# Optimization experiments

Hardware: AMD Instinct MI355X
Metric: run time of the kernel (lower is better)

## Reference

```python
import jax, jax.numpy as jnp
import numpy as np

N_NODES = 100000
N_EDGES = 3200000
HIDDEN = 64
OUT = 30


def _graph_conv(x, src, dst, W, b, n_nodes):
    # DGL GraphConv with norm='both': D_out^{-1/2} -> aggregate -> D_in^{-1/2} -> W -> +b
    ones = jnp.ones(src.shape[0], dtype=x.dtype)
    deg_out = jax.ops.segment_sum(ones, src, num_segments=n_nodes)
    deg_in = jax.ops.segment_sum(ones, dst, num_segments=n_nodes)
    norm_out = jnp.where(deg_out > 0, jax.lax.rsqrt(jnp.maximum(deg_out, 1e-30)), 0.0)
    norm_in = jnp.where(deg_in > 0, jax.lax.rsqrt(jnp.maximum(deg_in, 1e-30)), 0.0)
    h = x * norm_out[:, None]                    # [N, F] scaled source features
    msg = h[src]                                 # [E, F] gather
    agg = jax.ops.segment_sum(msg, dst, num_segments=n_nodes)  # [N, F] scatter-add
    agg = agg * norm_in[:, None]
    return agg @ W + b


def setup_inputs() -> dict:
    key = jax.random.key(0)
    k1, k2, k3, k4, k5 = jax.random.split(key, 5)
    x = jax.random.normal(k1, (N_NODES, HIDDEN), dtype=jnp.float32)
    src = jax.random.randint(k2, (N_EDGES,), 0, N_NODES, dtype=jnp.int32)
    dst = jax.random.randint(k3, (N_EDGES,), 0, N_NODES, dtype=jnp.int32)
    W1 = jax.random.normal(k4, (HIDDEN, HIDDEN), dtype=jnp.float32) / np.sqrt(HIDDEN)
    b1 = jnp.zeros((HIDDEN,), dtype=jnp.float32)
    W2 = jax.random.normal(k5, (HIDDEN, OUT), dtype=jnp.float32) / np.sqrt(HIDDEN)
    b2 = jnp.zeros((OUT,), dtype=jnp.float32)
    return {"x": x, "src": src, "dst": dst, "W1": W1, "b1": b1, "W2": W2, "b2": b2}


def reference(x, src, dst, W1, b1, W2, b2):
    h = _graph_conv(x, src, dst, W1, b1, N_NODES)
    h = jax.nn.relu(h)                           # conv1 activation=F.relu
    out = _graph_conv(h, src, dst, W2, b2, N_NODES)  # conv2: no activation
    return out
```

## Files before the change

kernel.cpp:

```cpp
#include <hip/hip_runtime.h>


#define NN 100000
#define NE 3200000
#define NOUTF 30
#define TPB 256
#define TPBW 1024
#define TPBS 1024

#define DSH 7
#define DCB 128
#define DNB ((NN + DCB - 1) / DCB)
#define SSH 8
#define SCB 256
#define SNB ((NN + SCB - 1) / SCB)

#define CHUNK 8192
#define NBLK ((NE + CHUNK - 1) / CHUNK)
#define HLD (DNB * NBLK)
#define HLS (SNB * NBLK)
#define HLT (HLD + HLS)
#define EPT (CHUNK / TPBS)

#define GCH 1024
#define NSC ((HLT + GCH - 1) / GCH)

#define POOL 4608

__device__ __forceinline__ unsigned short f2bf(float f) {
  unsigned u = __float_as_uint(f);
  u = (u + 0x7FFFu + ((u >> 16) & 1u)) >> 16;
  return (unsigned short)u;
}

__device__ __forceinline__ void acc8(float* a, const uint4& u) {
  a[0] += __uint_as_float(u.x << 16);
  a[1] += __uint_as_float(u.x & 0xFFFF0000u);
  a[2] += __uint_as_float(u.y << 16);
  a[3] += __uint_as_float(u.y & 0xFFFF0000u);
  a[4] += __uint_as_float(u.z << 16);
  a[5] += __uint_as_float(u.z & 0xFFFF0000u);
  a[6] += __uint_as_float(u.w << 16);
  a[7] += __uint_as_float(u.w & 0xFFFF0000u);
}

__device__ __forceinline__ int xcd_swz(int orig, int n) {
  int q = n / 8, r = n % 8;
  int xcd = orig % 8, idx = orig / 8;
  return (xcd < r ? xcd * (q + 1) : r * (q + 1) + (xcd - r) * q) + idx;
}

__global__ __launch_bounds__(TPBW) void k_hist(const int* __restrict__ src,
                                               const int* __restrict__ dst,
                                               int* __restrict__ H) {
  __shared__ int hd[DNB], hs[SNB];
  int t = threadIdx.x, k = blockIdx.x;
  for (int b = t; b < DNB; b += TPBW) hd[b] = 0;
  for (int b = t; b < SNB; b += TPBW) hs[b] = 0;
  __syncthreads();
  int beg = k * CHUNK, end = min(NE, beg + CHUNK);
  for (int i = beg + t; i < end; i += TPBW) {
    atomicAdd(&hd[dst[i] >> DSH], 1);
    atomicAdd(&hs[src[i] >> SSH], 1);
  }
  __syncthreads();
  for (int b = t; b < DNB; b += TPBW) H[b * NBLK + k] = hd[b];
  for (int b = t; b < SNB; b += TPBW) H[HLD + b * NBLK + k] = hs[b];
}

__global__ __launch_bounds__(TPB) void g_scan1(const int* __restrict__ a,
                                               int* __restrict__ bsums) {
  int t = threadIdx.x;
  int base = blockIdx.x * GCH + t * 4;
  int s = 0;
#pragma unroll
  for (int j = 0; j < 4; ++j) { int idx = base + j; if (idx < HLT) s += a[idx]; }
  __shared__ int red[TPB];
  red[t] = s; __syncthreads();
  for (int off = TPB / 2; off > 0; off >>= 1) {
    if (t < off) red[t] += red[t + off];
    __syncthreads();
  }
  if (t == 0) bsums[blockIdx.x] = red[0];
}

__global__ __launch_bounds__(1024) void g_scan2(int* __restrict__ bsums) {
  int t = threadIdx.x;
  __shared__ int lds[1024];
  int v = (t < NSC) ? bsums[t] : 0;
  int acc = v; lds[t] = acc; __syncthreads();
  for (int off = 1; off < 1024; off <<= 1) {
    int add = (t >= off) ? lds[t - off] : 0; __syncthreads();
    acc += add; lds[t] = acc; __syncthreads();
  }
  if (t < NSC) bsums[t] = acc - v;
}

__global__ __launch_bounds__(TPB) void g_scan3(int* __restrict__ a,
                                               const int* __restrict__ bsums) {
  int t = threadIdx.x;
  int base = blockIdx.x * GCH + t * 4;
  int v[4]; int s = 0;
#pragma unroll
  for (int j = 0; j < 4; ++j) {
    int idx = base + j;
    v[j] = (idx < HLT) ? a[idx] : 0;
    s += v[j];
  }
  __shared__ int lds[TPB];
  int acc = s; lds[t] = acc; __syncthreads();
  for (int off = 1; off < TPB; off <<= 1) {
    int add = (t >= off) ? lds[t - off] : 0; __syncthreads();
    acc += add; lds[t] = acc; __syncthreads();
  }
  int run = bsums[blockIdx.x] + (acc - s);
#pragma unroll
  for (int j = 0; j < 4; ++j) {
    int idx = base + j;
    if (idx < HLT) a[idx] = run;
    run += v[j];
  }
}

__global__ __launch_bounds__(TPBS) void k_scatter(const int* __restrict__ src,
                                                  const int* __restrict__ dst,
                                                  const int* __restrict__ Hsc,
                                                  int* __restrict__ packed,
                                                  unsigned char* __restrict__ ss) {
  __shared__ unsigned short perm_d[CHUNK];
  __shared__ unsigned short perm_s[CHUNK];
  __shared__ int baseD[DNB + 1], curD[DNB];
  __shared__ int baseS[SNB + 1], curS[SNB];
  __shared__ int scanbuf[TPBS];
  int t = threadIdx.x;
  int k = xcd_swz((int)blockIdx.x, NBLK);
  int beg = k * CHUNK, end = min(NE, beg + CHUNK);
  int cnt = end - beg;

  int es[EPT], ed[EPT];
#pragma unroll
  for (int j = 0; j < EPT; ++j) {
    int i = beg + j * TPBS + t;
    if (i < end) { es[j] = src[i]; ed[j] = dst[i]; }
    else { es[j] = -1; ed[j] = -1; }
  }

  for (int b = t; b < DNB; b += TPBS) curD[b] = 0;
  for (int b = t; b < SNB; b += TPBS) curS[b] = 0;
  __syncthreads();
#pragma unroll
  for (int j = 0; j < EPT; ++j) {
    if (ed[j] >= 0) {
      atomicAdd(&curD[ed[j] >> DSH], 1);
      atomicAdd(&curS[es[j] >> SSH], 1);
    }
  }
  __syncthreads();

  {
    int v = (t < DNB) ? curD[t] : 0;
    int acc = v; scanbuf[t] = acc; __syncthreads();
    for (int off = 1; off < TPBS; off <<= 1) {
      int add = (t >= off) ? scanbuf[t - off] : 0; __syncthreads();
      acc += add; scanbuf[t] = acc; __syncthreads();
    }
    if (t < DNB) baseD[t] = acc - v;
    if (t == 0) baseD[DNB] = cnt;
  }
  __syncthreads();
  {
    int v = (t < SNB) ? curS[t] : 0;
    int acc = v; scanbuf[t] = acc; __syncthreads();
    for (int off = 1; off < TPBS; off <<= 1) {
      int add = (t >= off) ? scanbuf[t - off] : 0; __syncthreads();
      acc += add; scanbuf[t] = acc; __syncthreads();
    }
    if (t < SNB) baseS[t] = acc - v;
    if (t == 0) baseS[SNB] = cnt;
  }
  __syncthreads();
  for (int b = t; b < DNB; b += TPBS) curD[b] = baseD[b];
  for (int b = t; b < SNB; b += TPBS) curS[b] = baseS[b];
  __syncthreads();

#pragma unroll
  for (int j = 0; j < EPT; ++j) {
    if (ed[j] >= 0) {
      int li = j * TPBS + t;
      int p = atomicAdd(&curD[ed[j] >> DSH], 1);
      perm_d[p] = (unsigned short)li;
      int q = atomicAdd(&curS[es[j] >> SSH], 1);
      perm_s[q] = (unsigned short)li;
    }
  }
  __syncthreads();

  for (int i = t; i < cnt; i += TPBS) {
    int gi = beg + perm_d[i];
    int d = dst[gi], s = src[gi];
    int bkt = d >> DSH;
    packed[Hsc[bkt * NBLK + k] + (i - baseD[bkt])] = (s << DSH) | (d & (DCB - 1));
  }
  for (int i = t; i < cnt; i += TPBS) {
    int gi = beg + perm_s[i];
    int s = src[gi];
    int bkt = s >> SSH;
    ss[Hsc[HLD + bkt * NBLK + k] + (i - baseS[bkt]) - NE] = (unsigned char)(s & (SCB - 1));
  }
}

__global__ __launch_bounds__(TPB) void k_fine_sort(const int* __restrict__ Hsc,
                                                   const int* __restrict__ packed,
                                                   int* __restrict__ src_sorted,
                                                   int* __restrict__ row_ptr,
                                                   float* __restrict__ norm_in) {
  __shared__ int hist[DCB], scn[DCB], cur[DCB];
  __shared__ int pool[POOL];
  int t = threadIdx.x, b = blockIdx.x;
  int seg_beg = Hsc[b * NBLK];
  int seg_end = (b + 1 < DNB) ? Hsc[(b + 1) * NBLK] : NE;
  int cnt = seg_end - seg_beg;
  if (t < DCB) hist[t] = 0;
  __syncthreads();
  for (int i = seg_beg + t; i < seg_end; i += TPB)
    atomicAdd(&hist[packed[i] & (DCB - 1)], 1);
  __syncthreads();
  if (t < DCB) scn[t] = hist[t];
  __syncthreads();
  for (int off = 1; off < DCB; off <<= 1) {
    int add = (t >= off && t < DCB) ? scn[t - off] : 0;
    __syncthreads();
    if (t < DCB) scn[t] += add;
    __syncthreads();
  }
  if (t < DCB) {
    int excl = scn[t] - hist[t];
    cur[t] = excl;
    int node = b * DCB + t;
    if (node < NN) {
      row_ptr[node] = seg_beg + excl;
      norm_in[node] = (hist[t] > 0) ? rsqrtf((float)hist[t]) : 0.0f;
    }
  }
  if (b == DNB - 1 && t == 0) row_ptr[NN] = NE;
  __syncthreads();
  for (int i = seg_beg + t; i < seg_end; i += TPB) {
    int v = packed[i];
    int p = atomicAdd(&cur[v & (DCB - 1)], 1);
    int sv = v >> DSH;
    if (p < POOL) pool[p] = sv;
    else src_sorted[seg_beg + p] = sv;
  }
  __syncthreads();
  int lim = min(cnt, POOL);
  for (int i = t; i < lim; i += TPB) src_sorted[seg_beg + i] = pool[i];
}

__global__ __launch_bounds__(TPB) void k_fine_count(const int* __restrict__ Hsc,
                                                    const unsigned char* __restrict__ ss,
                                                    float* __restrict__ norm_out) {
  __shared__ int hist[SCB];
  int t = threadIdx.x, b = blockIdx.x;
  int seg_beg = Hsc[HLD + b * NBLK] - NE;
  int seg_end = (b + 1 < SNB) ? Hsc[HLD + (b + 1) * NBLK] - NE : NE;
  if (t < SCB) hist[t] = 0;
  __syncthreads();
  for (int i = seg_beg + t; i < seg_end; i += TPB)
    atomicAdd(&hist[ss[i]], 1);
  __syncthreads();
  if (t < SCB) {
    int node = b * SCB + t;
    if (node < NN)
      norm_out[node] = (hist[t] > 0) ? rsqrtf((float)hist[t]) : 0.0f;
  }
}

__global__ __launch_bounds__(TPB) void k_gemm1(const float4* __restrict__ x4,
                                               const float* __restrict__ W1,
                                               const float* __restrict__ norm_out,
                                               unsigned short* __restrict__ xt_b) {
  int lane = threadIdx.x & 63;
  int wid = (blockIdx.x * TPB + threadIdx.x) >> 6;
  int nwaves = gridDim.x * (TPB / 64);
  float w[64];
#pragma unroll
  for (int k = 0; k < 64; ++k) w[k] = W1[k * 64 + lane];
  int m = lane >> 4, q = lane & 15;
  for (int grp = wid; grp < NN / 4; grp += nwaves) {
    int nbase = grp * 4;
    float4 rv = x4[(nbase + m) * 16 + q];
    int r0 = __float_as_int(rv.x), r1 = __float_as_int(rv.y);
    int r2 = __float_as_int(rv.z), r3 = __float_as_int(rv.w);
    float acc[4] = {0.f, 0.f, 0.f, 0.f};
#pragma unroll
    for (int mm = 0; mm < 4; ++mm) {
#pragma unroll
      for (int ql = 0; ql < 16; ++ql) {
        int sl = mm * 16 + ql;
        acc[mm] = fmaf(__int_as_float(__builtin_amdgcn_readlane(r0, sl)), w[ql * 4 + 0], acc[mm]);
        acc[mm] = fmaf(__int_as_float(__builtin_amdgcn_readlane(r1, sl)), w[ql * 4 + 1], acc[mm]);
        acc[mm] = fmaf(__int_as_float(__builtin_amdgcn_readlane(r2, sl)), w[ql * 4 + 2], acc[mm]);
        acc[mm] = fmaf(__int_as_float(__builtin_amdgcn_readlane(r3, sl)), w[ql * 4 + 3], acc[mm]);
      }
    }
#pragma unroll
    for (int mm = 0; mm < 4; ++mm) {
      int n = nbase + mm;
      xt_b[n * 64 + lane] = f2bf(norm_out[n] * acc[mm]);
    }
  }
}

__global__ __launch_bounds__(TPB) void k_agg1(const uint4* __restrict__ xt4,
                                              const int* __restrict__ src_sorted,
                                              const int* __restrict__ row_ptr,
                                              const float* __restrict__ norm_in,
                                              const float* __restrict__ b1,
                                              uint4* __restrict__ h1_b4) {
  int node = (blockIdx.x * TPB + threadIdx.x) >> 6;
  int lane = threadIdx.x & 63;
  int slot = lane >> 3;
  int fl = lane & 7;
  int beg = row_ptr[node];
  int end = row_ptr[node + 1];
  float a[8] = {0.f, 0.f, 0.f, 0.f, 0.f, 0.f, 0.f, 0.f};
  int e = beg + slot;
  for (; e + 8 < end; e += 16) {
    int s0 = src_sorted[e];
    int s1 = src_sorted[e + 8];
    uint4 u0 = xt4[s0 * 8 + fl];
    uint4 u1 = xt4[s1 * 8 + fl];
    acc8(a, u0);
    acc8(a, u1);
  }
  if (e < end) {
    uint4 u0 = xt4[src_sorted[e] * 8 + fl];
    acc8(a, u0);
  }
#pragma unroll
  for (int off = 8; off <= 32; off <<= 1) {
#pragma unroll
    for (int j = 0; j < 8; ++j) a[j] += __shfl_xor(a[j], off);
  }
  if (slot == 0) {
    float ni = norm_in[node];
    const float4* b1_4 = reinterpret_cast<const float4*>(b1);
    float4 bl = b1_4[fl * 2];
    float4 bh = b1_4[fl * 2 + 1];
    float v0 = fmaxf(fmaf(a[0], ni, bl.x), 0.f);
    float v1 = fmaxf(fmaf(a[1], ni, bl.y), 0.f);
    float v2 = fmaxf(fmaf(a[2], ni, bl.z), 0.f);
    float v3 = fmaxf(fmaf(a[3], ni, bl.w), 0.f);
    float v4 = fmaxf(fmaf(a[4], ni, bh.x), 0.f);
    float v5 = fmaxf(fmaf(a[5], ni, bh.y), 0.f);
    float v6 = fmaxf(fmaf(a[6], ni, bh.z), 0.f);
    float v7 = fmaxf(fmaf(a[7], ni, bh.w), 0.f);
    uint4 o;
    o.x = (unsigned)f2bf(v0) | ((unsigned)f2bf(v1) << 16);
    o.y = (unsigned)f2bf(v2) | ((unsigned)f2bf(v3) << 16);
    o.z = (unsigned)f2bf(v4) | ((unsigned)f2bf(v5) << 16);
    o.w = (unsigned)f2bf(v6) | ((unsigned)f2bf(v7) << 16);
    h1_b4[node * 8 + fl] = o;
  }
}

__global__ __launch_bounds__(TPB) void k_gemm2b(const uint4* __restrict__ h1b4,
                                                const float* __restrict__ W2,
                                                const float* __restrict__ norm_out,
                                                unsigned short* __restrict__ h1t_b) {
  int lane = threadIdx.x & 63;
  int wid = (blockIdx.x * TPB + threadIdx.x) >> 6;
  int nwaves = gridDim.x * (TPB / 64);
  int oc = lane & 31;
  float w[64];
#pragma unroll
  for (int k = 0; k < 64; ++k)
    w[k] = (oc < NOUTF) ? W2[k * NOUTF + oc] : 0.f;
  int r = lane >> 3, q = lane & 7;
  for (int grp = wid; grp < NN / 8; grp += nwaves) {
    int nbase = grp * 8;
    uint4 rv = h1b4[(nbase + r) * 8 + q];
    int v0 = (int)rv.x, v1 = (int)rv.y, v2 = (int)rv.z, v3 = (int)rv.w;
#pragma unroll
    for (int rr = 0; rr < 8; ++rr) {
      float acc0 = 0.f, acc1 = 0.f;
#pragma unroll
      for (int qq = 0; qq < 8; ++qq) {
        int sl = rr * 8 + qq;
        unsigned u0 = (unsigned)__builtin_amdgcn_readlane(v0, sl);
        unsigned u1 = (unsigned)__builtin_amdgcn_readlane(v1, sl);
        unsigned u2 = (unsigned)__builtin_amdgcn_readlane(v2, sl);
        unsigned u3 = (unsigned)__builtin_amdgcn_readlane(v3, sl);
        acc0 = fmaf(__uint_as_float(u0 << 16),          w[qq * 8 + 0], acc0);
        acc1 = fmaf(__uint_as_float(u0 & 0xFFFF0000u), w[qq * 8 + 1], acc1);
        acc0 = fmaf(__uint_as_float(u1 << 16),          w[qq * 8 + 2], acc0);
        acc1 = fmaf(__uint_as_float(u1 & 0xFFFF0000u), w[qq * 8 + 3], acc1);
        acc0 = fmaf(__uint_as_float(u2 << 16),          w[qq * 8 + 4], acc0);
        acc1 = fmaf(__uint_as_float(u2 & 0xFFFF0000u), w[qq * 8 + 5], acc1);
        acc0 = fmaf(__uint_as_float(u3 << 16),          w[qq * 8 + 6], acc0);
        acc1 = fmaf(__uint_as_float(u3 & 0xFFFF0000u), w[qq * 8 + 7], acc1);
      }
      int n = nbase + rr;
      if (lane < 32) {
        float acc = acc0 + acc1;
        unsigned short hv = (oc < NOUTF) ? f2bf(norm_out[n] * acc) : (unsigned short)0;
        h1t_b[n * 32 + oc] = hv;
      }
    }
  }
}

__global__ __launch_bounds__(TPB) void k_agg2(const uint4* __restrict__ h1t4,
                                              const int* __restrict__ src_sorted,
                                              const int* __restrict__ row_ptr,
                                              const float* __restrict__ norm_in,
                                              const float* __restrict__ b2,
                                              float* __restrict__ out) {
  int node = (blockIdx.x * TPB + threadIdx.x) >> 6;
  int lane = threadIdx.x & 63;
  int slot = lane >> 2;
  int fl = lane & 3;
  int beg = row_ptr[node];
  int end = row_ptr[node + 1];
  float a[8] = {0.f, 0.f, 0.f, 0.f, 0.f, 0.f, 0.f, 0.f};
  int e = beg + slot;
  for (; e + 16 < end; e += 32) {
    int s0 = src_sorted[e];
    int s1 = src_sorted[e + 16];
    uint4 u0 = h1t4[s0 * 4 + fl];
    uint4 u1 = h1t4[s1 * 4 + fl];
    acc8(a, u0);
    acc8(a, u1);
  }
  if (e < end) {
    uint4 u0 = h1t4[src_sorted[e] * 4 + fl];
    acc8(a, u0);
  }
#pragma unroll
  for (int off = 4; off <= 32; off <<= 1) {
#pragma unroll
    for (int j = 0; j < 8; ++j) a[j] += __shfl_xor(a[j], off);
  }
  if (slot == 0) {
    float ni = norm_in[node];
    int f0 = fl * 8;
    float2* ob = (float2*)(out + (size_t)node * NOUTF);
#pragma unroll
    for (int p = 0; p < 4; ++p) {
      int f = f0 + p * 2;
      if (f < NOUTF) {
        float2 v;
        v.x = fmaf(a[p * 2], ni, b2[f]);
        v.y = fmaf(a[p * 2 + 1], ni, b2[f + 1]);
        ob[f >> 1] = v;
      }
    }
  }
}

extern "C" void kernel_launch(void* const* d_in, const int* in_sizes, int n_in,
                              void* d_out, int out_size, void* d_ws, size_t ws_size,
                              hipStream_t stream) {
  (void)in_sizes; (void)n_in; (void)out_size; (void)ws_size;
  const float* x = (const float*)d_in[0];
  const int* src = (const int*)d_in[1];
  const int* dst = (const int*)d_in[2];
  const float* W1 = (const float*)d_in[3];
  const float* b1 = (const float*)d_in[4];
  const float* W2 = (const float*)d_in[5];
  const float* b2 = (const float*)d_in[6];
  float* out = (float*)d_out;

  char* ws = (char*)d_ws;
  int* row_ptr = (int*)(ws + 0);
  float* norm_out = (float*)(ws + 400128);
  float* norm_in = (float*)(ws + 800128);
  int* H = (int*)(ws + 1200128);
  int* bsums = (int*)(ws + 3100128);
  unsigned char* ss = (unsigned char*)(ws + 3101952);
  int* src_sorted = (int*)(ws + 8365696);
  int* packed = (int*)(ws + 21165696);
  uint4* h1_b4 = (uint4*)(ws + 21165696);
  unsigned short* xt_b = (unsigned short*)(ws + 46765696);
  unsigned short* h1t_b = (unsigned short*)(ws + 46765696);

  k_hist<<<NBLK, TPBW, 0, stream>>>(src, dst, H);
  g_scan1<<<NSC, TPB, 0, stream>>>(H, bsums);
  g_scan2<<<1, 1024, 0, stream>>>(bsums);
  g_scan3<<<NSC, TPB, 0, stream>>>(H, bsums);
  k_scatter<<<NBLK, TPBS, 0, stream>>>(src, dst, H, packed, ss);
  k_fine_sort<<<DNB, TPB, 0, stream>>>(H, packed, src_sorted, row_ptr, norm_in);
  k_fine_count<<<SNB, TPB, 0, stream>>>(H, ss, norm_out);
  k_gemm1<<<1024, TPB, 0, stream>>>((const float4*)x, W1, norm_out, xt_b);
  k_agg1<<<NN / 4, TPB, 0, stream>>>((const uint4*)xt_b, src_sorted, row_ptr,
                                     norm_in, b1, h1_b4);
  k_gemm2b<<<1024, TPB, 0, stream>>>((const uint4*)h1_b4, W2, norm_out, h1t_b);
  k_agg2<<<NN / 4, TPB, 0, stream>>>((const uint4*)h1t_b, src_sorted, row_ptr, norm_in, b2, out);
}
```

Before: 245.5 us.

## Fuse scan stages and fine kernels, reuse global histogram in scatter

The single-block block-sum scan is folded into the final scan kernel, with each block redundantly scanning the small block-sum array. The scatter kernel derives per-chunk bucket offsets from the already-scanned global histogram instead of recomputing local histograms with LDS atomics. The fine sort and fine count kernels are merged into one launch that branches on block index. These changes cut launch count and redundant atomic work, at the cost of some redundant scan work in every block.

```diff
diff --git a/kernel.cpp b/kernel.cpp
--- a/kernel.cpp
+++ b/kernel.cpp
@@ -20,7 +20,6 @@
 #define HLD (DNB * NBLK)
 #define HLS (SNB * NBLK)
 #define HLT (HLD + HLS)
-#define EPT (CHUNK / TPBS)
 
 #define GCH 1024
 #define NSC ((HLT + GCH - 1) / GCH)
@@ -84,21 +83,28 @@
   if (t == 0) bsums[blockIdx.x] = red[0];
 }
 
-__global__ __launch_bounds__(1024) void g_scan2(int* __restrict__ bsums) {
-  int t = threadIdx.x;
-  __shared__ int lds[1024];
-  int v = (t < NSC) ? bsums[t] : 0;
-  int acc = v; lds[t] = acc; __syncthreads();
-  for (int off = 1; off < 1024; off <<= 1) {
-    int add = (t >= off) ? lds[t - off] : 0; __syncthreads();
-    acc += add; lds[t] = acc; __syncthreads();
-  }
-  if (t < NSC) bsums[t] = acc - v;
-}
-
 __global__ __launch_bounds__(TPB) void g_scan3(int* __restrict__ a,
                                                const int* __restrict__ bsums) {
+  __shared__ int lds[TPB];
+  __shared__ int sc[512];
   int t = threadIdx.x;
+  {
+    int i0 = 2 * t, i1 = 2 * t + 1;
+    int v0 = (i0 < NSC) ? bsums[i0] : 0;
+    int v1 = (i1 < NSC) ? bsums[i1] : 0;
+    int s2 = v0 + v1;
+    int acc = s2; lds[t] = acc; __syncthreads();
+    for (int off = 1; off < TPB; off <<= 1) {
+      int add = (t >= off) ? lds[t - off] : 0; __syncthreads();
+      acc += add; lds[t] = acc; __syncthreads();
+    }
+    int excl = acc - s2;
+    sc[i0] = excl;
+    sc[i1] = excl + v0;
+  }
+  __syncthreads();
+  int pref = sc[blockIdx.x];
+  __syncthreads();
   int base = blockIdx.x * GCH + t * 4;
   int v[4]; int s = 0;
 #pragma unroll
@@ -107,13 +113,12 @@
     v[j] = (idx < HLT) ? a[idx] : 0;
     s += v[j];
   }
-  __shared__ int lds[TPB];
   int acc = s; lds[t] = acc; __syncthreads();
   for (int off = 1; off < TPB; off <<= 1) {
     int add = (t >= off) ? lds[t - off] : 0; __syncthreads();
     acc += add; lds[t] = acc; __syncthreads();
   }
-  int run = bsums[blockIdx.x] + (acc - s);
+  int run = pref + (acc - s);
 #pragma unroll
   for (int j = 0; j < 4; ++j) {
     int idx = base + j;
@@ -129,149 +134,134 @@
                                                   unsigned char* __restrict__ ss) {
   __shared__ unsigned short perm_d[CHUNK];
   __shared__ unsigned short perm_s[CHUNK];
-  __shared__ int baseD[DNB + 1], curD[DNB];
-  __shared__ int baseS[SNB + 1], curS[SNB];
+  __shared__ int curD[DNB], adjD[DNB];
+  __shared__ int curS[SNB], adjS[SNB];
   __shared__ int scanbuf[TPBS];
   int t = threadIdx.x;
   int k = xcd_swz((int)blockIdx.x, NBLK);
   int beg = k * CHUNK, end = min(NE, beg + CHUNK);
   int cnt = end - beg;
 
-  int es[EPT], ed[EPT];
-#pragma unroll
-  for (int j = 0; j < EPT; ++j) {
-    int i = beg + j * TPBS + t;
-    if (i < end) { es[j] = src[i]; ed[j] = dst[i]; }
-    else { es[j] = -1; ed[j] = -1; }
-  }
-
-  for (int b = t; b < DNB; b += TPBS) curD[b] = 0;
-  for (int b = t; b < SNB; b += TPBS) curS[b] = 0;
-  __syncthreads();
-#pragma unroll
-  for (int j = 0; j < EPT; ++j) {
-    if (ed[j] >= 0) {
-      atomicAdd(&curD[ed[j] >> DSH], 1);
-      atomicAdd(&curS[es[j] >> SSH], 1);
-    }
-  }
-  __syncthreads();
-
   {
-    int v = (t < DNB) ? curD[t] : 0;
-    int acc = v; scanbuf[t] = acc; __syncthreads();
+    int st = 0, c = 0;
+    if (t < DNB) {
+      int idx = t * NBLK + k;
+      st = Hsc[idx];
+      int en = (idx + 1 < HLT) ? Hsc[idx + 1] : 2 * NE;
+      c = en - st;
+    }
+    int acc = c; scanbuf[t] = acc; __syncthreads();
     for (int off = 1; off < TPBS; off <<= 1) {
       int add = (t >= off) ? scanbuf[t - off] : 0; __syncthreads();
       acc += add; scanbuf[t] = acc; __syncthreads();
     }
-    if (t < DNB) baseD[t] = acc - v;
-    if (t == 0) baseD[DNB] = cnt;
+    int excl = acc - c;
+    if (t < DNB) { curD[t] = excl; adjD[t] = st - excl; }
   }
   __syncthreads();
   {
-    int v = (t < SNB) ? curS[t] : 0;
-    int acc = v; scanbuf[t] = acc; __syncthreads();
+    int st = 0, c = 0;
+    if (t < SNB) {
+      int idx = HLD + t * NBLK + k;
+      st = Hsc[idx];
+      int en = (idx + 1 < HLT) ? Hsc[idx + 1] : 2 * NE;
+      c = en - st;
+    }
+    int acc = c; scanbuf[t] = acc; __syncthreads();
     for (int off = 1; off < TPBS; off <<= 1) {
       int add = (t >= off) ? scanbuf[t - off] : 0; __syncthreads();
       acc += add; scanbuf[t] = acc; __syncthreads();
     }
-    if (t < SNB) baseS[t] = acc - v;
-    if (t == 0) baseS[SNB] = cnt;
-  }
-  __syncthreads();
-  for (int b = t; b < DNB; b += TPBS) curD[b] = baseD[b];
-  for (int b = t; b < SNB; b += TPBS) curS[b] = baseS[b];
-  __syncthreads();
-
-#pragma unroll
-  for (int j = 0; j < EPT; ++j) {
-    if (ed[j] >= 0) {
-      int li = j * TPBS + t;
-      int p = atomicAdd(&curD[ed[j] >> DSH], 1);
-      perm_d[p] = (unsigned short)li;
-      int q = atomicAdd(&curS[es[j] >> SSH], 1);
-      perm_s[q] = (unsigned short)li;
-    }
+    int excl = acc - c;
+    if (t < SNB) { curS[t] = excl; adjS[t] = (st - NE) - excl; }
+  }
+  __syncthreads();
+
+  for (int i = beg + t; i < end; i += TPBS) {
+    int s = src[i], d = dst[i];
+    int li = i - beg;
+    int p = atomicAdd(&curD[d >> DSH], 1);
+    perm_d[p] = (unsigned short)li;
+    int q = atomicAdd(&curS[s >> SSH], 1);
+    perm_s[q] = (unsigned short)li;
   }
   __syncthreads();
 
   for (int i = t; i < cnt; i += TPBS) {
     int gi = beg + perm_d[i];
     int d = dst[gi], s = src[gi];
-    int bkt = d >> DSH;
-    packed[Hsc[bkt * NBLK + k] + (i - baseD[bkt])] = (s << DSH) | (d & (DCB - 1));
+    packed[adjD[d >> DSH] + i] = (s << DSH) | (d & (DCB - 1));
   }
   for (int i = t; i < cnt; i += TPBS) {
-    int gi = beg + perm_s[i];
-    int s = src[gi];
-    int bkt = s >> SSH;
-    ss[Hsc[HLD + bkt * NBLK + k] + (i - baseS[bkt]) - NE] = (unsigned char)(s & (SCB - 1));
-  }
-}
-
-__global__ __launch_bounds__(TPB) void k_fine_sort(const int* __restrict__ Hsc,
-                                                   const int* __restrict__ packed,
-                                                   int* __restrict__ src_sorted,
-                                                   int* __restrict__ row_ptr,
-                                                   float* __restrict__ norm_in) {
+    int s = src[beg + perm_s[i]];
+    ss[adjS[s >> SSH] + i] = (unsigned char)(s & (SCB - 1));
+  }
+}
+
+__global__ __launch_bounds__(TPB) void k_fine(const int* __restrict__ Hsc,
+                                              const int* __restrict__ packed,
+                                              const unsigned char* __restrict__ ss,
+                                              int* __restrict__ src_sorted,
+                                              int* __restrict__ row_ptr,
+                                              float* __restrict__ norm_in,
+                                              float* __restrict__ norm_out) {
   __shared__ int hist[DCB], scn[DCB], cur[DCB];
   __shared__ int pool[POOL];
-  int t = threadIdx.x, b = blockIdx.x;
-  int seg_beg = Hsc[b * NBLK];
-  int seg_end = (b + 1 < DNB) ? Hsc[(b + 1) * NBLK] : NE;
-  int cnt = seg_end - seg_beg;
-  if (t < DCB) hist[t] = 0;
-  __syncthreads();
-  for (int i = seg_beg + t; i < seg_end; i += TPB)
-    atomicAdd(&hist[packed[i] & (DCB - 1)], 1);
-  __syncthreads();
-  if (t < DCB) scn[t] = hist[t];
-  __syncthreads();
-  for (int off = 1; off < DCB; off <<= 1) {
-    int add = (t >= off && t < DCB) ? scn[t - off] : 0;
-    __syncthreads();
-    if (t < DCB) scn[t] += add;
-    __syncthreads();
-  }
-  if (t < DCB) {
-    int excl = scn[t] - hist[t];
-    cur[t] = excl;
-    int node = b * DCB + t;
-    if (node < NN) {
-      row_ptr[node] = seg_beg + excl;
-      norm_in[node] = (hist[t] > 0) ? rsqrtf((float)hist[t]) : 0.0f;
-    }
-  }
-  if (b == DNB - 1 && t == 0) row_ptr[NN] = NE;
-  __syncthreads();
-  for (int i = seg_beg + t; i < seg_end; i += TPB) {
-    int v = packed[i];
-    int p = atomicAdd(&cur[v & (DCB - 1)], 1);
-    int sv = v >> DSH;
-    if (p < POOL) pool[p] = sv;
-    else src_sorted[seg_beg + p] = sv;
-  }
-  __syncthreads();
-  int lim = min(cnt, POOL);
-  for (int i = t; i < lim; i += TPB) src_sorted[seg_beg + i] = pool[i];
-}
-
-__global__ __launch_bounds__(TPB) void k_fine_count(const int* __restrict__ Hsc,
-                                                    const unsigned char* __restrict__ ss,
-                                                    float* __restrict__ norm_out) {
-  __shared__ int hist[SCB];
-  int t = threadIdx.x, b = blockIdx.x;
-  int seg_beg = Hsc[HLD + b * NBLK] - NE;
-  int seg_end = (b + 1 < SNB) ? Hsc[HLD + (b + 1) * NBLK] - NE : NE;
-  if (t < SCB) hist[t] = 0;
-  __syncthreads();
-  for (int i = seg_beg + t; i < seg_end; i += TPB)
-    atomicAdd(&hist[ss[i]], 1);
-  __syncthreads();
-  if (t < SCB) {
-    int node = b * SCB + t;
-    if (node < NN)
-      norm_out[node] = (hist[t] > 0) ? rsqrtf((float)hist[t]) : 0.0f;
+  __shared__ int histS[SCB];
+  int t = threadIdx.x;
+  if (blockIdx.x < DNB) {
+    int b = blockIdx.x;
+    int seg_beg = Hsc[b * NBLK];
+    int seg_end = (b + 1 < DNB) ? Hsc[(b + 1) * NBLK] : NE;
+    int cnt = seg_end - seg_beg;
+    if (t < DCB) hist[t] = 0;
+    __syncthreads();
+    for (int i = seg_beg + t; i < seg_end; i += TPB)
+      atomicAdd(&hist[packed[i] & (DCB - 1)], 1);
+    __syncthreads();
+    if (t < DCB) scn[t] = hist[t];
+    __syncthreads();
+    for (int off = 1; off < DCB; off <<= 1) {
+      int add = (t >= off && t < DCB) ? scn[t - off] : 0;
+      __syncthreads();
+      if (t < DCB) scn[t] += add;
+      __syncthreads();
+    }
+    if (t < DCB) {
+      int excl = scn[t] - hist[t];
+      cur[t] = excl;
+      int node = b * DCB + t;
+      if (node < NN) {
+        row_ptr[node] = seg_beg + excl;
+        norm_in[node] = (hist[t] > 0) ? rsqrtf((float)hist[t]) : 0.0f;
+      }
+    }
+    if (b == DNB - 1 && t == 0) row_ptr[NN] = NE;
+    __syncthreads();
+    for (int i = seg_beg + t; i < seg_end; i += TPB) {
+      int v = packed[i];
+      int p = atomicAdd(&cur[v & (DCB - 1)], 1);
+      int sv = v >> DSH;
+      if (p < POOL) pool[p] = sv;
+      else src_sorted[seg_beg + p] = sv;
+    }
+    __syncthreads();
+    int lim = min(cnt, POOL);
+    for (int i = t; i < lim; i += TPB) src_sorted[seg_beg + i] = pool[i];
+  } else {
+    int b = blockIdx.x - DNB;
+    int seg_beg = Hsc[HLD + b * NBLK] - NE;
+    int seg_end = (b + 1 < SNB) ? Hsc[HLD + (b + 1) * NBLK] - NE : NE;
+    if (t < SCB) histS[t] = 0;
+    __syncthreads();
+    for (int i = seg_beg + t; i < seg_end; i += TPB)
+      atomicAdd(&histS[ss[i]], 1);
+    __syncthreads();
+    if (t < SCB) {
+      int node = b * SCB + t;
+      if (node < NN)
+        norm_out[node] = (histS[t] > 0) ? rsqrtf((float)histS[t]) : 0.0f;
+    }
   }
 }
 
@@ -486,11 +476,9 @@
 
   k_hist<<<NBLK, TPBW, 0, stream>>>(src, dst, H);
   g_scan1<<<NSC, TPB, 0, stream>>>(H, bsums);
-  g_scan2<<<1, 1024, 0, stream>>>(bsums);
   g_scan3<<<NSC, TPB, 0, stream>>>(H, bsums);
   k_scatter<<<NBLK, TPBS, 0, stream>>>(src, dst, H, packed, ss);
-  k_fine_sort<<<DNB, TPB, 0, stream>>>(H, packed, src_sorted, row_ptr, norm_in);
-  k_fine_count<<<SNB, TPB, 0, stream>>>(H, ss, norm_out);
+  k_fine<<<DNB + SNB, TPB, 0, stream>>>(H, packed, ss, src_sorted, row_ptr, norm_in, norm_out);
   k_gemm1<<<1024, TPB, 0, stream>>>((const float4*)x, W1, norm_out, xt_b);
   k_agg1<<<NN / 4, TPB, 0, stream>>>((const uint4*)xt_b, src_sorted, row_ptr,
                                      norm_in, b1, h1_b4);
```

After: 231.7 us. 1.06x faster.
